# Optimization experiments

Measured on AMD Instinct MI355X. Metric: run time of the kernel, lower is better.

## Reference

```python
import jax, jax.numpy as jnp
import numpy as np

B, MAX_LEN, V, H, E = 256, 31, 10000, 512, 512


def setup_inputs() -> dict:
    key = jax.random.key(0)
    ks = jax.random.split(key, 10)
    s = 0.05
    return {
        "global_images": jax.random.normal(ks[0], (B, E), jnp.float32),
        "w_input": jax.random.randint(ks[1], (B, MAX_LEN), 0, V),
        "caption_lengths": jax.random.randint(ks[2], (B,), 2, MAX_LEN + 1),
        "emb": jax.random.normal(ks[3], (V, E), jnp.float32) * s,
        "W_ih": jax.random.normal(ks[4], (4 * H, 2 * E), jnp.float32) * s,
        "W_hh": jax.random.normal(ks[5], (4 * H, H), jnp.float32) * s,
        "b_ih": jax.random.normal(ks[6], (4 * H,), jnp.float32) * s,
        "b_hh": jax.random.normal(ks[7], (4 * H,), jnp.float32) * s,
        "W_out": jax.random.normal(ks[8], (V, H), jnp.float32) * s,
        "b_out": jax.random.normal(ks[9], (V,), jnp.float32) * s,
    }


def reference(global_images, w_input, caption_lengths, emb, W_ih, W_hh, b_ih, b_hh, W_out, b_out):
    # Sort by caption length, descending (mirrors torch .sort(descending=True))
    order = jnp.argsort(-caption_lengths)
    lens = caption_lengths[order]
    w = w_input[order]                      # [B, max_len]
    g = global_images[order]                # [B, E]
    target = w[:, 1:]                       # [B, max_len-1]
    dec_len = lens - 1                      # has_end_seq_token=True

    T = w.shape[1] - 1                      # max decode steps
    h0 = jnp.zeros((g.shape[0], W_hh.shape[1]), dtype=g.dtype)
    c0 = jnp.zeros_like(h0)
    words = w[:, :T].T                      # [T, B]
    ts = jnp.arange(T)

    def step(carry, inp):
        h, c = carry
        w_t, t = inp
        x_t = jnp.concatenate([g, emb[w_t]], axis=1)          # [B, 2E]
        gates = x_t @ W_ih.T + b_ih + h @ W_hh.T + b_hh       # [B, 4H]
        i, f, gg, o = jnp.split(gates, 4, axis=1)
        i, f, o = jax.nn.sigmoid(i), jax.nn.sigmoid(f), jax.nn.sigmoid(o)
        gg = jnp.tanh(gg)
        c_new = f * c + i * gg
        h_new = o * jnp.tanh(c_new)
        active = (t < dec_len)[:, None]                       # shrinking active batch
        h = jnp.where(active, h_new, h)
        c = jnp.where(active, c_new, c)
        pt = jax.nn.log_softmax(h_new @ W_out.T + b_out, axis=1)
        pt = jnp.where(active, pt, jnp.zeros((), pt.dtype))
        return (h, c), pt

    (_, _), preds = jax.lax.scan(step, (h0, c0), (words, ts))
    preds = jnp.transpose(preds, (1, 0, 2))                   # [B, T, V]
    preds = jnp.pad(preds, ((0, 0), (0, 1), (0, 0)))          # -> [B, max_len, V]
    return preds, target, dec_len
```

## Files before the change

kernel.cpp:

```cpp
#include <hip/hip_runtime.h>
#include <hip/hip_bf16.h>
#include <math.h>

#define NB   256
#define ML   31
#define NT   30
#define NV   10000
#define NH   512
#define NE   512
#define NG   2048

#define OFF_TGT  (256LL*31LL*10000LL)
#define OFF_DEC  (OFF_TGT + 256LL*30LL)
#define PRED_B   (31LL*10000LL)

typedef __attribute__((ext_vector_type(8))) short bf16x8;
typedef __attribute__((ext_vector_type(4))) float f32x4;

__device__ inline unsigned short f2bf(float f) {
    unsigned int x = __float_as_uint(f);
    unsigned int r = x + 0x7FFFu + ((x >> 16) & 1u);
    return (unsigned short)(r >> 16);
}
__device__ inline float bf2f(unsigned short u) {
    return __uint_as_float((unsigned int)u << 16);
}

__device__ inline void gl2lds16(const void* g, void* l) {
    __builtin_amdgcn_global_load_lds(
        (const __attribute__((address_space(1))) unsigned int*)g,
        (__attribute__((address_space(3))) unsigned int*)l, 16, 0, 0);
}

__global__ void sort_k(const int* __restrict__ lens, int* __restrict__ order,
                       int* __restrict__ cnt, int* __restrict__ start,
                       int* __restrict__ flags, float* __restrict__ out_dec) {
    __shared__ int sd[NB];
    int i = threadIdx.x;
    flags[i] = 0;
    int li = lens[i];
    int r = 0;
    for (int j = 0; j < NB; j++) {
        int lj = lens[j];
        r += (lj > li) || (lj == li && j < i);
    }
    order[r] = i;
    out_dec[r] = (float)(li - 1);
    sd[r] = li - 1;
    __syncthreads();
    if (i < NT) {
        int c = 0;
        for (int b = 0; b < NB; b++) c += (sd[b] > i);
        cnt[i] = c;
    }
    __syncthreads();
    if (i == 0) {
        int s = 0;
        for (int t = 0; t < NT; t++) { start[t] = s; s += cnt[t]; }
        start[NT] = s;
    }
}

__global__ void gather_k(const float* __restrict__ gimg, const int* __restrict__ w_in,
                         const int* __restrict__ order,
                         unsigned short* __restrict__ g_sb, int* __restrict__ wsort,
                         float* __restrict__ out_tgt) {
    int r = blockIdx.x, tid = threadIdx.x;
    int o = order[r];
    for (int e = tid; e < NE; e += 256)
        g_sb[r * NE + e] = f2bf(gimg[o * NE + e]);
    if (tid < ML) wsort[r * ML + tid] = w_in[o * ML + tid];
    if (tid < NT) out_tgt[r * NT + tid] = (float)w_in[o * ML + tid + 1];
}

__global__ void rowlist_k(const int* __restrict__ wsort, const int* __restrict__ cnt,
                          const int* __restrict__ start,
                          int* __restrict__ rowlist, int* __restrict__ rowwc,
                          float* __restrict__ rowsum) {
    int t = blockIdx.x, b = threadIdx.x;
    rowsum[t * 256 + b] = 0.f;
    if (b < cnt[t]) {
        int pos = start[t] + b;
        rowlist[pos] = t * 256 + b;
        rowwc[pos] = wsort[b * ML + t];
    }
}

__global__ void prep_k(const float* __restrict__ W_ih, const float* __restrict__ W_hh,
                       const float* __restrict__ W_out, const float* __restrict__ emb,
                       unsigned short* __restrict__ Wxl, unsigned short* __restrict__ Wxb,
                       unsigned short* __restrict__ Wob, unsigned short* __restrict__ embb,
                       unsigned short* __restrict__ Wimg2) {
    int bid = blockIdx.x, tid = threadIdx.x;
    if (bid < 2048) {
        int koff = (bid < 1024) ? 0 : NE;
        unsigned short* dst = (bid < 1024) ? Wxl : Wxb;
        int gid = ((bid & 1023) << 8) + tid;
        int j = gid >> 7, k4 = gid & 127;
        float4 v = *(const float4*)(W_ih + (size_t)j * (2 * NE) + koff + k4 * 4);
        ushort4 o;
        o.x = f2bf(v.x); o.y = f2bf(v.y); o.z = f2bf(v.z); o.w = f2bf(v.w);
        *(ushort4*)(dst + (size_t)j * NE + k4 * 4) = o;
    } else if (bid < 12048) {
        const float* src = (bid < 7048) ? W_out : emb;
        unsigned short* dst = (bid < 7048) ? Wob : embb;
        int gid = ((bid < 7048 ? bid - 2048 : bid - 7048) << 8) + tid;
        float4 v = ((const float4*)src)[gid];
        ushort4 o;
        o.x = f2bf(v.x); o.y = f2bf(v.y); o.z = f2bf(v.z); o.w = f2bf(v.w);
        ((ushort4*)dst)[gid] = o;
    } else {
        int gid = ((bid - 12048) << 8) + tid;
        int hi = gid & 3, kt = (gid >> 2) & 15, R = (gid >> 6) & 127, s = gid >> 13;
        int q = R >> 5, ct = (R >> 4) & 1, lo = R & 15;
        int col = q * 512 + s * 32 + ct * 16 + lo;
        int k = kt * 32 + hi * 8;
        const float* src = W_hh + (size_t)col * NH + k;
        __align__(16) unsigned short o[8];
#pragma unroll
        for (int j = 0; j < 8; ++j) o[j] = f2bf(src[j]);
        int ba = (R << 10) + ((kt * 64 + hi * 16) ^ ((lo & 7) << 4));
        *(uint4*)((char*)Wimg2 + ((size_t)s << 17) + ba) = *(const uint4*)o;
    }
}

__launch_bounds__(256)
__global__ void gxgemm(const unsigned short* __restrict__ Abf,
                       const unsigned short* __restrict__ Bbf,
                       const float* __restrict__ bias1, const float* __restrict__ bias2,
                       float* __restrict__ outf) {
    __shared__ __align__(16) char Bs[131072];
    int m0 = blockIdx.y * 128, n0 = blockIdx.x * 128;
    int tid = threadIdx.x;
    int lane = tid & 63, w = tid >> 6;
    int wy = w >> 1, wx = w & 1;

#pragma unroll 4
    for (int p = 0; p < 32; ++p) {
        int row = (tid >> 6) + (p << 2);
        uint4 v = *(const uint4*)(Bbf + ((size_t)(n0 + row) << 9) + ((tid & 63) << 3));
        int ba = (row << 10) + ((tid & 63) << 4); ba ^= (row & 7) << 4;
        *(uint4*)(Bs + ba) = v;
    }
    const unsigned short* aptr[4];
#pragma unroll
    for (int rt = 0; rt < 4; ++rt)
        aptr[rt] = Abf + ((size_t)(m0 + (wy << 6) + (rt << 4) + (lane & 15)) << 9);

    f32x4 acc[4][4];
#pragma unroll
    for (int i = 0; i < 4; ++i)
#pragma unroll
        for (int j = 0; j < 4; ++j) acc[i][j] = (f32x4){0.f, 0.f, 0.f, 0.f};
    __syncthreads();

#pragma unroll 4
    for (int ks = 0; ks < 16; ++ks) {
        int koff = (ks << 5) + ((lane >> 4) << 3);
        bf16x8 bq[4];
#pragma unroll
        for (int ct = 0; ct < 4; ++ct) {
            int brow = (wx << 6) + (ct << 4) + (lane & 15);
            int bb = (brow << 10) + (koff << 1); bb ^= (brow & 7) << 4;
            bq[ct] = *(const bf16x8*)(Bs + bb);
        }
#pragma unroll
        for (int rt = 0; rt < 4; ++rt) {
            bf16x8 aq = *(const bf16x8*)(aptr[rt] + koff);
#pragma unroll
            for (int ct = 0; ct < 4; ++ct)
                acc[rt][ct] = __builtin_amdgcn_mfma_f32_16x16x32_bf16(aq, bq[ct], acc[rt][ct], 0, 0, 0);
        }
    }
#pragma unroll
    for (int rt = 0; rt < 4; ++rt)
#pragma unroll
        for (int ct = 0; ct < 4; ++ct) {
            int n = n0 + (wx << 6) + (ct << 4) + (lane & 15);
            float badd = bias1[n] + bias2[n];
#pragma unroll
            for (int ri = 0; ri < 4; ++ri) {
                int m = m0 + (wy << 6) + (rt << 4) + ((lane >> 4) << 2) + ri;
                outf[(size_t)m * NG + n] = acc[rt][ct][ri] + badd;
            }
        }
}

template <int AMODE, int EPI>
__launch_bounds__(256)
__global__ void pgemm(const unsigned short* __restrict__ Abf,
                      const int* __restrict__ ridx,
                      const unsigned short* __restrict__ Aemb,
                      const unsigned short* __restrict__ Bbf,
                      int N,
                      const int* __restrict__ mact_p,
                      const float* __restrict__ bias1,
                      const int* __restrict__ rowlist,
                      unsigned short* __restrict__ outb,
                      float* __restrict__ rowsum) {
    __shared__ __align__(16) char lds[65536];
    int Mact = *mact_p;
    int m0 = blockIdx.x * 128;
    if (m0 >= Mact) return;
    int n0 = blockIdx.y * 128;
    int tid = threadIdx.x;
    int lane = tid & 63, w = tid >> 6;
    int wy = w >> 1, wx = w & 1;
    int hi = lane >> 4, lo = lane & 15;

    const char* asrc[4];
#pragma unroll
    for (int i = 0; i < 4; ++i) {
        int p = (i << 8) + tid;
        int ma = m0 + (p >> 3); if (ma > Mact - 1) ma = Mact - 1;
        if (AMODE == 0) asrc[i] = (const char*)Abf + ((size_t)ma << 10);
        else            asrc[i] = (const char*)Aemb + ((size_t)ridx[ma] << 10);
    }

    auto stage = [&](int kt, int buf) {
#pragma unroll
        for (int i = 0; i < 4; ++i) {
            int p = (i << 8) + tid;
            int row = p >> 3, sc = (p & 7) ^ (row & 7);
            gl2lds16(asrc[i] + (kt << 7) + (sc << 4), lds + (buf << 14) + (p << 4));
        }
#pragma unroll
        for (int i = 0; i < 4; ++i) {
            int p = (i << 8) + tid;
            int row = p >> 3, sc = (p & 7) ^ (row & 7);
            int nb = n0 + row; if (nb > N - 1) nb = N - 1;
            gl2lds16((const char*)Bbf + ((size_t)nb << 10) + (kt << 7) + (sc << 4),
                     lds + 32768 + (buf << 14) + (p << 4));
        }
    };

    f32x4 acc[4][4];
#pragma unroll
    for (int i = 0; i < 4; ++i)
#pragma unroll
        for (int j = 0; j < 4; ++j) acc[i][j] = (f32x4){0.f, 0.f, 0.f, 0.f};

    stage(0, 0);
    __syncthreads();

    for (int kt = 0; kt < 8; ++kt) {
        int buf = kt & 1;
        if (kt < 7) stage(kt + 1, buf ^ 1);
#pragma unroll
        for (int kc = 0; kc < 2; ++kc) {
            bf16x8 aq[4], bq[4];
#pragma unroll
            for (int rt = 0; rt < 4; ++rt) {
                int ra = (wy << 6) + (rt << 4) + lo;
                int cha = ((kc << 2) + hi) ^ (ra & 7);
                aq[rt] = *(const bf16x8*)(lds + (buf << 14) + (ra << 7) + (cha << 4));
                int cb = (wx << 6) + (rt << 4) + lo;
                int chb = ((kc << 2) + hi) ^ (cb & 7);
                bq[rt] = *(const bf16x8*)(lds + 32768 + (buf << 14) + (cb << 7) + (chb << 4));
            }
#pragma unroll
            for (int rt = 0; rt < 4; ++rt)
#pragma unroll
                for (int ct = 0; ct < 4; ++ct)
                    acc[rt][ct] = __builtin_amdgcn_mfma_f32_16x16x32_bf16(aq[rt], bq[ct], acc[rt][ct], 0, 0, 0);
        }
        __syncthreads();
    }

    if (EPI == 0) {
#pragma unroll
        for (int rt = 0; rt < 4; ++rt)
#pragma unroll
            for (int ct = 0; ct < 4; ++ct) {
                int n = n0 + (wx << 6) + (ct << 4) + lo;
#pragma unroll
                for (int ri = 0; ri < 4; ++ri) {
                    int m = m0 + (wy << 6) + (rt << 4) + (hi << 2) + ri;
                    if (m < Mact) {
                        int b = rowlist[m] & 255;
                        float v = acc[rt][ct][ri] + bias1[(size_t)b * NG + n];
                        outb[(size_t)m * NG + ((n & 511) << 2) + (n >> 9)] = f2bf(v);
                    }
                }
            }
    } else {
#pragma unroll
        for (int rt = 0; rt < 4; ++rt) {
            float es4[4] = {0.f, 0.f, 0.f, 0.f};
#pragma unroll
            for (int ct = 0; ct < 4; ++ct) {
                int n = n0 + (wx << 6) + (ct << 4) + lo;
                bool okn = (n < N);
                float bo = okn ? bias1[n] : 0.f;
#pragma unroll
                for (int ri = 0; ri < 4; ++ri) {
                    int m = m0 + (wy << 6) + (rt << 4) + (hi << 2) + ri;
                    float v = acc[rt][ct][ri] + bo;
                    if (okn && m < Mact) {
                        outb[(size_t)m * NV + n] = f2bf(v);
                        es4[ri] += __expf(v);
                    }
                }
            }
#pragma unroll
            for (int ri = 0; ri < 4; ++ri) {
                float s = es4[ri];
                s += __shfl_xor(s, 1); s += __shfl_xor(s, 2);
                s += __shfl_xor(s, 4); s += __shfl_xor(s, 8);
                if (lo == 0) {
                    int m = m0 + (wy << 6) + (rt << 4) + (hi << 2) + ri;
                    if (m < Mact) atomicAdd(&rowsum[m], s);
                }
            }
        }
    }
}

__launch_bounds__(256, 1)
__global__ void lstmy_k(const unsigned short* __restrict__ Wimg2,
                        const unsigned short* __restrict__ gallc,
                        unsigned short* __restrict__ hx,
                        unsigned short* __restrict__ h_allc,
                        int* __restrict__ flags,
                        const int* __restrict__ cnt,
                        const int* __restrict__ start) {
    __shared__ __align__(16) char Wlds[131072];
    __shared__ float Gs[4 * 16 * 32];
    __shared__ __align__(16) unsigned short hstg[16 * 32];
    int tid = threadIdx.x;
    int g = blockIdx.x & 15, s = blockIdx.x >> 4;
    int lane = tid & 63, w = tid >> 6;
    int hi = lane >> 4, lo = lane & 15;
    int q = w;

    {
        const char* wsrc = (const char*)Wimg2 + ((size_t)s << 17) + tid * 16;
#pragma unroll 8
        for (int r = 0; r < 32; ++r)
            gl2lds16(wsrc + r * 4096, Wlds + tid * 16 + r * 4096);
    }
    asm volatile("s_waitcnt vmcnt(0)" ::: "memory");
    __syncthreads();

    int row = tid >> 4, d0 = tid & 15;
    float creg[2] = {0.f, 0.f};

    for (int t = 0; t < NT; ++t) {
        int cnt_t = cnt[t];
        if (16 * g >= cnt_t) break;
        int nrow = cnt_t - 16 * g; if (nrow > 16) nrow = 16;
        int pos0 = start[t] + 16 * g;

        int rr = row < nrow ? row : nrow - 1;
        const unsigned short* gp = gallc + ((size_t)(pos0 + rr) << 11);
        uint2 gq0 = *(const uint2*)(gp + (s * 32 + d0) * 4);
        uint2 gq1 = *(const uint2*)(gp + (s * 32 + d0 + 16) * 4);

        f32x4 acc[2];
        acc[0] = (f32x4){0.f, 0.f, 0.f, 0.f};
        acc[1] = (f32x4){0.f, 0.f, 0.f, 0.f};

        if (t > 0) {
            {
                const int* fp = flags + g * 16 + lo;
                int f;
                do {
                    asm volatile("global_load_dword %0, %1, off sc0 sc1\n\t"
                                 "s_waitcnt vmcnt(0)"
                                 : "=v"(f) : "v"(fp) : "memory");
                } while (__any(f < t));
            }
            const char* hb = (const char*)hx +
                ((size_t)(((t - 1) & 1) * 16 + g) << 14) + (lo << 6) + (hi << 4);
            uint4 hv[16];
#pragma unroll
            for (int c = 0; c < 16; ++c)
                asm volatile("global_load_dwordx4 %0, %1, off sc0 sc1"
                             : "=v"(hv[c]) : "v"(hb + (c << 10)) : "memory");
            asm volatile("s_waitcnt vmcnt(0)" ::: "memory");
            __builtin_amdgcn_sched_barrier(0);
#pragma unroll
            for (int kt = 0; kt < 16; ++kt) {
                bf16x8 aq = *(const bf16x8*)&hv[kt];
#pragma unroll
                for (int ct = 0; ct < 2; ++ct) {
                    int R = (q * 2 + ct) * 16 + lo;
                    int bb = (R << 10) + ((kt * 64 + hi * 16) ^ ((lo & 7) << 4));
                    bf16x8 bq = *(const bf16x8*)(Wlds + bb);
                    acc[ct] = __builtin_amdgcn_mfma_f32_16x16x32_bf16(aq, bq, acc[ct], 0, 0, 0);
                }
            }
        }
#pragma unroll
        for (int ct = 0; ct < 2; ++ct)
#pragma unroll
            for (int ri = 0; ri < 4; ++ri)
                Gs[(q * 16 + hi * 4 + ri) * 32 + ct * 16 + lo] = acc[ct][ri];
        __syncthreads();

        bool act = row < nrow;
#pragma unroll
        for (int p = 0; p < 2; ++p) {
            int dp = d0 + p * 16;
            const unsigned short* gq = (const unsigned short*)(p ? &gq1 : &gq0);
            float iv = Gs[(0 * 16 + row) * 32 + dp] + bf2f(gq[0]);
            float fv = Gs[(1 * 16 + row) * 32 + dp] + bf2f(gq[1]);
            float gv = Gs[(2 * 16 + row) * 32 + dp] + bf2f(gq[2]);
            float ov = Gs[(3 * 16 + row) * 32 + dp] + bf2f(gq[3]);
            float i_ = 1.f / (1.f + __expf(-iv));
            float f_ = 1.f / (1.f + __expf(-fv));
            float o_ = 1.f / (1.f + __expf(-ov));
            float ea = __expf(-2.f * fabsf(gv));
            float th = (1.f - ea) / (1.f + ea);
            th = (gv < 0.f) ? -th : th;
            float cn = f_ * creg[p] + i_ * th;
            float ec = __expf(-2.f * fabsf(cn));
            float tc = (1.f - ec) / (1.f + ec);
            tc = (cn < 0.f) ? -tc : tc;
            float hn = o_ * tc;
            unsigned short hv16;
            if (act) {
                creg[p] = cn;
                hv16 = f2bf(hn);
            } else {
                hv16 = hstg[row * 32 + dp];
            }
            hstg[row * 32 + dp] = hv16;
        }
        __syncthreads();

        uint2 v0, v1;
        int crow = tid >> 2, j = tid & 3;
        if (tid < 64) {
            v0 = *(const uint2*)(hstg + crow * 32 + j * 8);
            v1 = *(const uint2*)(hstg + crow * 32 + j * 8 + 4);
            char* himg = (char*)hx + ((size_t)((t & 1) * 16 + g) << 14);
            int dstoff = (s << 10) + (crow << 6) + (j << 4);
            asm volatile("global_store_dwordx2 %0, %2, off sc0 sc1\n\t"
                         "global_store_dwordx2 %1, %3, off sc0 sc1"
                         :: "v"(himg + dstoff), "v"(himg + dstoff + 8),
                            "v"(v0), "v"(v1) : "memory");
        }
        asm volatile("s_waitcnt vmcnt(0)" ::: "memory");
        __syncthreads();
        if (tid == 0) {
            int fv = t + 1;
            asm volatile("global_store_dword %0, %1, off sc0 sc1"
                         :: "v"(flags + g * 16 + s), "v"(fv) : "memory");
        }
        if (tid < 64 && crow < nrow) {
            unsigned short* hap = h_allc + (size_t)(pos0 + crow) * NH + s * 32 + j * 8;
            *(uint2*)hap = v0;
            *(uint2*)(hap + 4) = v1;
        }
    }
}

__global__ void norm_k(float* __restrict__ out, const unsigned short* __restrict__ logitb,
                       const float* __restrict__ rowsum,
                       const int* __restrict__ cnt, const int* __restrict__ start) {
    int r = blockIdx.x;
    int t = r >> 8, b = r & 255;
    bool act = (t < NT) && (b < cnt[t]);
    float4* row = (float4*)(out + (size_t)b * PRED_B + (size_t)t * NV);
    int tid = threadIdx.x;
    if (act) {
        int pos = start[t] + b;
        float lse = logf(rowsum[pos]);
        const uint4* lrow = (const uint4*)(logitb + (size_t)pos * NV);
        for (int v8 = tid; v8 < NV / 8; v8 += 256) {
            uint4 u = lrow[v8];
            float4 a, c;
            a.x = bf2f((unsigned short)u.x) - lse;
            a.y = bf2f((unsigned short)(u.x >> 16)) - lse;
            a.z = bf2f((unsigned short)u.y) - lse;
            a.w = bf2f((unsigned short)(u.y >> 16)) - lse;
            c.x = bf2f((unsigned short)u.z) - lse;
            c.y = bf2f((unsigned short)(u.z >> 16)) - lse;
            c.z = bf2f((unsigned short)u.w) - lse;
            c.w = bf2f((unsigned short)(u.w >> 16)) - lse;
            row[v8 * 2] = a;
            row[v8 * 2 + 1] = c;
        }
    } else {
        float4 z = make_float4(0.f, 0.f, 0.f, 0.f);
        for (int v4 = tid; v4 < NV / 4; v4 += 256) row[v4] = z;
    }
}

extern "C" void kernel_launch(void* const* d_in, const int* in_sizes, int n_in,
                              void* d_out, int out_size, void* d_ws, size_t ws_size,
                              hipStream_t stream) {
    const float* gimg  = (const float*)d_in[0];
    const int*   w_in  = (const int*)d_in[1];
    const int*   lens  = (const int*)d_in[2];
    const float* emb   = (const float*)d_in[3];
    const float* W_ih  = (const float*)d_in[4];
    const float* W_hh  = (const float*)d_in[5];
    const float* b_ih  = (const float*)d_in[6];
    const float* b_hh  = (const float*)d_in[7];
    const float* W_out = (const float*)d_in[8];
    const float* b_out = (const float*)d_in[9];
    float* out = (float*)d_out;

    char* p = (char*)d_ws;
    auto alloc = [&](size_t bytes) -> char* {
        char* r = p;
        p += (bytes + 255) & ~(size_t)255;
        return r;
    };
    int*   order   = (int*)alloc(NB * 4);
    int*   wsort   = (int*)alloc(NB * ML * 4);
    int*   cnt     = (int*)alloc(NT * 4);
    int*   start   = (int*)alloc((NT + 1) * 4);
    int*   flags   = (int*)alloc(256 * 4);
    int*   rowlist = (int*)alloc((size_t)NT * NB * 4);
    int*   rowwc   = (int*)alloc((size_t)NT * NB * 4);
    float* gx      = (float*)alloc((size_t)NB * NG * 4);
    float* rowsum  = (float*)alloc((size_t)NT * NB * 4);
    unsigned short* g_sb   = (unsigned short*)alloc((size_t)NB * NE * 2);
    unsigned short* hx     = (unsigned short*)alloc((size_t)2 * 16 * 16384);
    unsigned short* h_allc = (unsigned short*)alloc((size_t)NT * NB * NH * 2);
    unsigned short* Wimg2  = (unsigned short*)alloc((size_t)NG * NH * 2);
    unsigned short* Wxl    = (unsigned short*)alloc((size_t)NG * NE * 2);
    unsigned short* Wxb    = (unsigned short*)alloc((size_t)NG * NE * 2);
    unsigned short* Wob    = (unsigned short*)alloc((size_t)NV * NH * 2);
    unsigned short* embb   = (unsigned short*)alloc((size_t)NV * NE * 2);
    unsigned short* gallc  = (unsigned short*)alloc((size_t)NT * NB * NG * 2);
    unsigned short* logitb = (unsigned short*)alloc((size_t)NT * NB * NV * 2);
    int* nact = start + NT;

    sort_k<<<1, 256, 0, stream>>>(lens, order, cnt, start, flags, out + OFF_DEC);
    gather_k<<<NB, 256, 0, stream>>>(gimg, w_in, order, g_sb, wsort, out + OFF_TGT);
    rowlist_k<<<NT, 256, 0, stream>>>(wsort, cnt, start, rowlist, rowwc, rowsum);
    prep_k<<<12560, 256, 0, stream>>>(W_ih, W_hh, W_out, emb, Wxl, Wxb, Wob, embb, Wimg2);

    gxgemm<<<dim3(NG / 128, NB / 128), 256, 0, stream>>>(g_sb, Wxl, b_ih, b_hh, gx);

    pgemm<1, 0><<<dim3(NT * NB / 128, NG / 128), 256, 0, stream>>>(
        nullptr, rowwc, embb, Wxb, NG, nact, gx, rowlist, gallc, nullptr);

    {
        void* cargs[] = { (void*)&Wimg2, (void*)&gallc, (void*)&hx, (void*)&h_allc,
                          (void*)&flags, (void*)&cnt, (void*)&start };
        (void)hipLaunchCooperativeKernel((void*)lstmy_k, dim3(256), dim3(256), cargs, 0, stream);
    }

    pgemm<0, 1><<<dim3(NT * NB / 128, (NV + 127) / 128), 256, 0, stream>>>(
        h_allc, nullptr, nullptr, Wob, NV, nact, b_out, rowlist, logitb, rowsum);

    norm_k<<<(NT + 1) * NB, 256, 0, stream>>>(out, logitb, rowsum, cnt, start);
}
```

Before: 423.9 us.

## Fuse output-projection GEMM into persistent LSTM kernel with flag-gated work queue

The separate output-projection GEMM launch is removed. Its tiles are now processed inside the cooperative LSTM kernel, where blocks pull tile indices from an atomic work queue. Before computing a tile, a block spin-waits on per-step flags until every hidden-state row that tile needs has been written. The aim is to overlap the large vocab GEMM with the serial recurrence tail and save a launch, at the cost of limiting the GEMM to 256 blocks at one block per CU, extra polling, and bypass-cache loads of A through registers.

```diff
diff --git a/kernel.cpp b/kernel.cpp
--- a/kernel.cpp
+++ b/kernel.cpp
@@ -9,6 +9,7 @@
 #define NH   512
 #define NE   512
 #define NG   2048
+#define NTILES_N 79
 
 #define OFF_TGT  (256LL*31LL*10000LL)
 #define OFF_DEC  (OFF_TGT + 256LL*30LL)
@@ -38,6 +39,7 @@
     __shared__ int sd[NB];
     int i = threadIdx.x;
     flags[i] = 0;
+    if (i == 0) flags[256] = 0;
     int li = lens[i];
     int r = 0;
     for (int j = 0; j < NB; j++) {
@@ -186,18 +188,14 @@
         }
 }
 
-template <int AMODE, int EPI>
 __launch_bounds__(256)
-__global__ void pgemm(const unsigned short* __restrict__ Abf,
-                      const int* __restrict__ ridx,
-                      const unsigned short* __restrict__ Aemb,
-                      const unsigned short* __restrict__ Bbf,
-                      int N,
-                      const int* __restrict__ mact_p,
-                      const float* __restrict__ bias1,
-                      const int* __restrict__ rowlist,
-                      unsigned short* __restrict__ outb,
-                      float* __restrict__ rowsum) {
+__global__ void pgemm10(const int* __restrict__ ridx,
+                        const unsigned short* __restrict__ Aemb,
+                        const unsigned short* __restrict__ Bbf,
+                        const int* __restrict__ mact_p,
+                        const float* __restrict__ gxf,
+                        const int* __restrict__ rowlist,
+                        unsigned short* __restrict__ outb) {
     __shared__ __align__(16) char lds[65536];
     int Mact = *mact_p;
     int m0 = blockIdx.x * 128;
@@ -213,8 +211,7 @@
     for (int i = 0; i < 4; ++i) {
         int p = (i << 8) + tid;
         int ma = m0 + (p >> 3); if (ma > Mact - 1) ma = Mact - 1;
-        if (AMODE == 0) asrc[i] = (const char*)Abf + ((size_t)ma << 10);
-        else            asrc[i] = (const char*)Aemb + ((size_t)ridx[ma] << 10);
+        asrc[i] = (const char*)Aemb + ((size_t)ridx[ma] << 10);
     }
 
     auto stage = [&](int kt, int buf) {
@@ -228,7 +225,7 @@
         for (int i = 0; i < 4; ++i) {
             int p = (i << 8) + tid;
             int row = p >> 3, sc = (p & 7) ^ (row & 7);
-            int nb = n0 + row; if (nb > N - 1) nb = N - 1;
+            int nb = n0 + row;
             gl2lds16((const char*)Bbf + ((size_t)nb << 10) + (kt << 7) + (sc << 4),
                      lds + 32768 + (buf << 14) + (p << 4));
         }
@@ -267,66 +264,39 @@
         __syncthreads();
     }
 
-    if (EPI == 0) {
-#pragma unroll
-        for (int rt = 0; rt < 4; ++rt)
-#pragma unroll
-            for (int ct = 0; ct < 4; ++ct) {
-                int n = n0 + (wx << 6) + (ct << 4) + lo;
-#pragma unroll
-                for (int ri = 0; ri < 4; ++ri) {
-                    int m = m0 + (wy << 6) + (rt << 4) + (hi << 2) + ri;
-                    if (m < Mact) {
-                        int b = rowlist[m] & 255;
-                        float v = acc[rt][ct][ri] + bias1[(size_t)b * NG + n];
-                        outb[(size_t)m * NG + ((n & 511) << 2) + (n >> 9)] = f2bf(v);
-                    }
-                }
-            }
-    } else {
-#pragma unroll
-        for (int rt = 0; rt < 4; ++rt) {
-            float es4[4] = {0.f, 0.f, 0.f, 0.f};
-#pragma unroll
-            for (int ct = 0; ct < 4; ++ct) {
-                int n = n0 + (wx << 6) + (ct << 4) + lo;
-                bool okn = (n < N);
-                float bo = okn ? bias1[n] : 0.f;
-#pragma unroll
-                for (int ri = 0; ri < 4; ++ri) {
-                    int m = m0 + (wy << 6) + (rt << 4) + (hi << 2) + ri;
-                    float v = acc[rt][ct][ri] + bo;
-                    if (okn && m < Mact) {
-                        outb[(size_t)m * NV + n] = f2bf(v);
-                        es4[ri] += __expf(v);
-                    }
-                }
-            }
+#pragma unroll
+    for (int rt = 0; rt < 4; ++rt)
+#pragma unroll
+        for (int ct = 0; ct < 4; ++ct) {
+            int n = n0 + (wx << 6) + (ct << 4) + lo;
 #pragma unroll
             for (int ri = 0; ri < 4; ++ri) {
-                float s = es4[ri];
-                s += __shfl_xor(s, 1); s += __shfl_xor(s, 2);
-                s += __shfl_xor(s, 4); s += __shfl_xor(s, 8);
-                if (lo == 0) {
-                    int m = m0 + (wy << 6) + (rt << 4) + (hi << 2) + ri;
-                    if (m < Mact) atomicAdd(&rowsum[m], s);
-                }
-            }
-        }
-    }
+                int m = m0 + (wy << 6) + (rt << 4) + (hi << 2) + ri;
+                if (m < Mact) {
+                    int b = rowlist[m] & 255;
+                    float v = acc[rt][ct][ri] + gxf[(size_t)b * NG + n];
+                    outb[(size_t)m * NG + ((n & 511) << 2) + (n >> 9)] = f2bf(v);
+                }
+            }
+        }
 }
 
 __launch_bounds__(256, 1)
-__global__ void lstmy_k(const unsigned short* __restrict__ Wimg2,
+__global__ void lstmw_k(const unsigned short* __restrict__ Wimg2,
                         const unsigned short* __restrict__ gallc,
                         unsigned short* __restrict__ hx,
                         unsigned short* __restrict__ h_allc,
                         int* __restrict__ flags,
                         const int* __restrict__ cnt,
-                        const int* __restrict__ start) {
+                        const int* __restrict__ start,
+                        const unsigned short* __restrict__ Wob,
+                        const float* __restrict__ bout,
+                        unsigned short* __restrict__ logitb,
+                        float* __restrict__ rowsum) {
     __shared__ __align__(16) char Wlds[131072];
     __shared__ float Gs[4 * 16 * 32];
     __shared__ __align__(16) unsigned short hstg[16 * 32];
+    __shared__ int wq;
     int tid = threadIdx.x;
     int g = blockIdx.x & 15, s = blockIdx.x >> 4;
     int lane = tid & 63, w = tid >> 6;
@@ -400,9 +370,9 @@
 
         bool act = row < nrow;
 #pragma unroll
-        for (int p = 0; p < 2; ++p) {
-            int dp = d0 + p * 16;
-            const unsigned short* gq = (const unsigned short*)(p ? &gq1 : &gq0);
+        for (int pp = 0; pp < 2; ++pp) {
+            int dp = d0 + pp * 16;
+            const unsigned short* gq = (const unsigned short*)(pp ? &gq1 : &gq0);
             float iv = Gs[(0 * 16 + row) * 32 + dp] + bf2f(gq[0]);
             float fv = Gs[(1 * 16 + row) * 32 + dp] + bf2f(gq[1]);
             float gv = Gs[(2 * 16 + row) * 32 + dp] + bf2f(gq[2]);
@@ -413,14 +383,14 @@
             float ea = __expf(-2.f * fabsf(gv));
             float th = (1.f - ea) / (1.f + ea);
             th = (gv < 0.f) ? -th : th;
-            float cn = f_ * creg[p] + i_ * th;
+            float cn = f_ * creg[pp] + i_ * th;
             float ec = __expf(-2.f * fabsf(cn));
             float tc = (1.f - ec) / (1.f + ec);
             tc = (cn < 0.f) ? -tc : tc;
             float hn = o_ * tc;
             unsigned short hv16;
             if (act) {
-                creg[p] = cn;
+                creg[pp] = cn;
                 hv16 = f2bf(hn);
             } else {
                 hv16 = hstg[row * 32 + dp];
@@ -429,17 +399,22 @@
         }
         __syncthreads();
 
-        uint2 v0, v1;
         int crow = tid >> 2, j = tid & 3;
         if (tid < 64) {
-            v0 = *(const uint2*)(hstg + crow * 32 + j * 8);
-            v1 = *(const uint2*)(hstg + crow * 32 + j * 8 + 4);
+            uint2 v0 = *(const uint2*)(hstg + crow * 32 + j * 8);
+            uint2 v1 = *(const uint2*)(hstg + crow * 32 + j * 8 + 4);
             char* himg = (char*)hx + ((size_t)((t & 1) * 16 + g) << 14);
             int dstoff = (s << 10) + (crow << 6) + (j << 4);
             asm volatile("global_store_dwordx2 %0, %2, off sc0 sc1\n\t"
                          "global_store_dwordx2 %1, %3, off sc0 sc1"
                          :: "v"(himg + dstoff), "v"(himg + dstoff + 8),
                             "v"(v0), "v"(v1) : "memory");
+            if (crow < nrow) {
+                unsigned short* hap = h_allc + (size_t)(pos0 + crow) * NH + s * 32 + j * 8;
+                asm volatile("global_store_dwordx2 %0, %2, off sc0 sc1\n\t"
+                             "global_store_dwordx2 %1, %3, off sc0 sc1"
+                             :: "v"(hap), "v"(hap + 4), "v"(v0), "v"(v1) : "memory");
+            }
         }
         asm volatile("s_waitcnt vmcnt(0)" ::: "memory");
         __syncthreads();
@@ -448,10 +423,149 @@
             asm volatile("global_store_dword %0, %1, off sc0 sc1"
                          :: "v"(flags + g * 16 + s), "v"(fv) : "memory");
         }
-        if (tid < 64 && crow < nrow) {
-            unsigned short* hap = h_allc + (size_t)(pos0 + crow) * NH + s * 32 + j * 8;
-            *(uint2*)hap = v0;
-            *(uint2*)(hap + 4) = v1;
+    }
+
+    {
+        char* glds = Wlds;
+        int Mact = start[NT];
+        int mtiles = (Mact + 127) >> 7;
+        int total = mtiles * NTILES_N;
+        int wyW = w >> 1, wxW = w & 1;
+
+        for (;;) {
+            if (tid == 0) wq = atomicAdd(flags + 256, 1);
+            __syncthreads();
+            int idx = wq;
+            if (idx >= total) break;
+            int tm = idx / NTILES_N;
+            int tn = idx - tm * NTILES_N;
+            int m0w = tm << 7, n0w = tn << 7;
+            int mEnd = m0w + 128; if (mEnd > Mact) mEnd = Mact;
+
+            if (tid < 16) {
+                bool ok;
+                do {
+                    ok = true;
+                    for (int t = 0; t < NT && ok; ++t) {
+                        int st = start[t], cn = cnt[t];
+                        int lo2 = st > m0w ? st : m0w;
+                        int hi2 = (st + cn < mEnd) ? (st + cn) : mEnd;
+                        if (lo2 < hi2) {
+                            int glo = (lo2 - st) >> 4, ghi = (hi2 - 1 - st) >> 4;
+                            for (int gg = glo; gg <= ghi; ++gg) {
+                                int f;
+                                asm volatile("global_load_dword %0, %1, off sc0 sc1\n\t"
+                                             "s_waitcnt vmcnt(0)"
+                                             : "=v"(f) : "v"(flags + gg * 16 + tid) : "memory");
+                                if (f < t + 1) { ok = false; break; }
+                            }
+                        }
+                    }
+                    if (!ok) __builtin_amdgcn_s_sleep(8);
+                } while (!ok);
+            }
+            __syncthreads();
+
+            f32x4 acc[4][4];
+#pragma unroll
+            for (int i = 0; i < 4; ++i)
+#pragma unroll
+                for (int jj = 0; jj < 4; ++jj) acc[i][jj] = (f32x4){0.f, 0.f, 0.f, 0.f};
+
+            uint4 areg[4];
+            auto issueA = [&](int kt) {
+#pragma unroll
+                for (int i = 0; i < 4; ++i) {
+                    int p = (i << 8) + tid;
+                    int rw = p >> 3, sc = (p & 7) ^ (rw & 7);
+                    int ma = m0w + rw; if (ma > Mact - 1) ma = Mact - 1;
+                    asm volatile("global_load_dwordx4 %0, %1, off sc0 sc1"
+                                 : "=v"(areg[i])
+                                 : "v"((const char*)h_allc + ((size_t)ma << 10) + (kt << 7) + (sc << 4))
+                                 : "memory");
+                }
+            };
+            auto issueB = [&](int kt, int buf) {
+#pragma unroll
+                for (int i = 0; i < 4; ++i) {
+                    int p = (i << 8) + tid;
+                    int rw = p >> 3, sc = (p & 7) ^ (rw & 7);
+                    int nb = n0w + rw; if (nb > NV - 1) nb = NV - 1;
+                    gl2lds16((const char*)Wob + ((size_t)nb << 10) + (kt << 7) + (sc << 4),
+                             glds + 32768 + (buf << 14) + (p << 4));
+                }
+            };
+            auto writeA = [&](int buf) {
+#pragma unroll
+                for (int i = 0; i < 4; ++i) {
+                    int p = (i << 8) + tid;
+                    *(uint4*)(glds + (buf << 14) + (p << 4)) = areg[i];
+                }
+            };
+
+            issueA(0); issueB(0, 0);
+            asm volatile("s_waitcnt vmcnt(0)" ::: "memory");
+            writeA(0);
+            __syncthreads();
+
+            for (int kt = 0; kt < 8; ++kt) {
+                int buf = kt & 1;
+                if (kt < 7) { issueA(kt + 1); issueB(kt + 1, buf ^ 1); }
+#pragma unroll
+                for (int kc = 0; kc < 2; ++kc) {
+                    bf16x8 aq[4], bq[4];
+#pragma unroll
+                    for (int rt = 0; rt < 4; ++rt) {
+                        int ra = (wyW << 6) + (rt << 4) + lo;
+                        int cha = ((kc << 2) + hi) ^ (ra & 7);
+                        aq[rt] = *(const bf16x8*)(glds + (buf << 14) + (ra << 7) + (cha << 4));
+                        int cb = (wxW << 6) + (rt << 4) + lo;
+                        int chb = ((kc << 2) + hi) ^ (cb & 7);
+                        bq[rt] = *(const bf16x8*)(glds + 32768 + (buf << 14) + (cb << 7) + (chb << 4));
+                    }
+#pragma unroll
+                    for (int rt = 0; rt < 4; ++rt)
+#pragma unroll
+                        for (int ct = 0; ct < 4; ++ct)
+                            acc[rt][ct] = __builtin_amdgcn_mfma_f32_16x16x32_bf16(aq[rt], bq[ct], acc[rt][ct], 0, 0, 0);
+                }
+                if (kt < 7) {
+                    asm volatile("s_waitcnt vmcnt(0)" ::: "memory");
+                    writeA(buf ^ 1);
+                }
+                __syncthreads();
+            }
+
+#pragma unroll
+            for (int rt = 0; rt < 4; ++rt) {
+                float es4[4] = {0.f, 0.f, 0.f, 0.f};
+#pragma unroll
+                for (int ct = 0; ct < 4; ++ct) {
+                    int n = n0w + (wxW << 6) + (ct << 4) + lo;
+                    bool okn = (n < NV);
+                    float bo = okn ? bout[n] : 0.f;
+#pragma unroll
+                    for (int ri = 0; ri < 4; ++ri) {
+                        int m = m0w + (wyW << 6) + (rt << 4) + (hi << 2) + ri;
+                        float v = acc[rt][ct][ri] + bo;
+                        if (okn && m < Mact) {
+                            logitb[(size_t)m * NV + n] = f2bf(v);
+                            es4[ri] += __expf(v);
+                        }
+                    }
+                }
+#pragma unroll
+                for (int ri = 0; ri < 4; ++ri) {
+                    float ssum = es4[ri];
+                    ssum += __shfl_xor(ssum, 1); ssum += __shfl_xor(ssum, 2);
+                    ssum += __shfl_xor(ssum, 4); ssum += __shfl_xor(ssum, 8);
+                    if (lo == 0) {
+                        int m = m0w + (wyW << 6) + (rt << 4) + (hi << 2) + ri;
+                        if (m < Mact) atomicAdd(&rowsum[m], ssum);
+                    }
+                }
+            }
+            __syncthreads();
         }
     }
 }
@@ -513,7 +627,7 @@
     int*   wsort   = (int*)alloc(NB * ML * 4);
     int*   cnt     = (int*)alloc(NT * 4);
     int*   start   = (int*)alloc((NT + 1) * 4);
-    int*   flags   = (int*)alloc(256 * 4);
+    int*   flags   = (int*)alloc(512 * 4);
     int*   rowlist = (int*)alloc((size_t)NT * NB * 4);
     int*   rowwc   = (int*)alloc((size_t)NT * NB * 4);
     float* gx      = (float*)alloc((size_t)NB * NG * 4);
@@ -537,17 +651,15 @@
 
     gxgemm<<<dim3(NG / 128, NB / 128), 256, 0, stream>>>(g_sb, Wxl, b_ih, b_hh, gx);
 
-    pgemm<1, 0><<<dim3(NT * NB / 128, NG / 128), 256, 0, stream>>>(
-        nullptr, rowwc, embb, Wxb, NG, nact, gx, rowlist, gallc, nullptr);
+    pgemm10<<<dim3(NT * NB / 128, NG / 128), 256, 0, stream>>>(
+        rowwc, embb, Wxb, nact, gx, rowlist, gallc);
 
     {
         void* cargs[] = { (void*)&Wimg2, (void*)&gallc, (void*)&hx, (void*)&h_allc,
-                          (void*)&flags, (void*)&cnt, (void*)&start };
-        (void)hipLaunchCooperativeKernel((void*)lstmy_k, dim3(256), dim3(256), cargs, 0, stream);
-    }
-
-    pgemm<0, 1><<<dim3(NT * NB / 128, (NV + 127) / 128), 256, 0, stream>>>(
-        h_allc, nullptr, nullptr, Wob, NV, nact, b_out, rowlist, logitb, rowsum);
+                          (void*)&flags, (void*)&cnt, (void*)&start,
+                          (void*)&Wob, (void*)&b_out, (void*)&logitb, (void*)&rowsum };
+        (void)hipLaunchCooperativeKernel((void*)lstmw_k, dim3(256), dim3(256), cargs, 0, stream);
+    }
 
     norm_k<<<(NT + 1) * NB, 256, 0, stream>>>(out, logitb, rowsum, cnt, start);
 }
```

Result: slower. 525.3 us (+23.9%).
